# Performance work log

Measured on AMD Instinct MI355X. Metric: run time of the kernel, lower is better.

## Reference

```python
import jax, jax.numpy as jnp
import numpy as np

B, H, W = 4, 256, 256
DIM = 180
NH = 6
WH, WW = 16, 16          # window size
BH, BW = 8, 8            # base window size
CH = DIM // (2 * NH)     # per-head dim = 15
SCALE = float(CH)        # note: divide by head_dim (not sqrt), as in source
RH, RW = WH // BH, WW // BW
R = RH * RW              # spatial reduction ratio = 4
L = WH * WW              # 256 tokens per window
BL = BH * BW             # 64 base tokens
POS_DIM = (DIM // 4) // 4  # 11


def _rel_index(Hs, Ws):
    coords = np.stack(np.meshgrid(np.arange(Hs), np.arange(Ws), indexing='ij')).reshape(2, -1)
    rel = (coords[:, :, None] - coords[:, None, :]).transpose(1, 2, 0)
    rel[..., 0] += Hs - 1
    rel[..., 1] += Ws - 1
    rel[..., 0] *= 2 * Ws - 1
    return rel.sum(-1)  # (L, L) int

RPI = _rel_index(WH, WW)


def _ln(x, g, b):
    mu = x.mean(-1, keepdims=True)
    var = ((x - mu) ** 2).mean(-1, keepdims=True)
    return (x - mu) / jnp.sqrt(var + 1e-5) * g + b


def _conv(x, w, b):  # x: NHWC, w: HWIO
    y = jax.lax.conv_general_dilated(x, w, (1, 1), 'SAME',
                                     dimension_numbers=('NHWC', 'HWIO', 'NHWC'))
    return y + b


def setup_inputs():
    key = jax.random.key(0)
    ks = jax.random.split(key, 12)
    def wgt(k, shape, s=0.05):
        return jax.random.normal(k, shape, jnp.float32) * s
    C5 = DIM // 5
    d = {}
    d['x'] = jax.random.normal(ks[0], (B, H, W, DIM), jnp.float32)
    d['dfe_c1_w'] = wgt(ks[1], (1, 1, DIM, C5)); d['dfe_c1_b'] = jnp.zeros((C5,), jnp.float32)
    d['dfe_c2_w'] = wgt(ks[2], (3, 3, C5, C5));  d['dfe_c2_b'] = jnp.zeros((C5,), jnp.float32)
    d['dfe_c3_w'] = wgt(ks[3], (1, 1, C5, DIM)); d['dfe_c3_b'] = jnp.zeros((DIM,), jnp.float32)
    d['dfe_lin_w'] = wgt(ks[4], (1, 1, DIM, DIM)); d['dfe_lin_b'] = jnp.zeros((DIM,), jnp.float32)
    d['sl_w'] = wgt(ks[5], (1, R), 0.5); d['sl_b'] = jnp.zeros((1,), jnp.float32)
    d['pos_proj_w'] = wgt(ks[6], (POS_DIM, 2), 0.1); d['pos_proj_b'] = jnp.zeros((POS_DIM,), jnp.float32)
    for i, kk in zip((1, 2), (ks[7], ks[8])):
        d['pos%d_ln_g' % i] = jnp.ones((POS_DIM,), jnp.float32)
        d['pos%d_ln_b' % i] = jnp.zeros((POS_DIM,), jnp.float32)
        d['pos%d_w' % i] = wgt(kk, (POS_DIM, POS_DIM), 0.1)
        d['pos%d_b' % i] = jnp.zeros((POS_DIM,), jnp.float32)
    d['pos3_ln_g'] = jnp.ones((POS_DIM,), jnp.float32)
    d['pos3_ln_b'] = jnp.zeros((POS_DIM,), jnp.float32)
    d['pos3_w'] = wgt(ks[9], (NH, POS_DIM), 0.1)
    d['pos3_b'] = jnp.zeros((NH,), jnp.float32)
    d['proj_w'] = wgt(ks[10], (DIM, DIM))
    d['proj_b'] = jnp.zeros((DIM,), jnp.float32)
    return d


def reference(x, dfe_c1_w, dfe_c1_b, dfe_c2_w, dfe_c2_b, dfe_c3_w, dfe_c3_b,
              dfe_lin_w, dfe_lin_b, sl_w, sl_b, pos_proj_w, pos_proj_b,
              pos1_ln_g, pos1_ln_b, pos1_w, pos1_b,
              pos2_ln_g, pos2_ln_b, pos2_w, pos2_b,
              pos3_ln_g, pos3_ln_b, pos3_w, pos3_b,
              proj_w, proj_b):
    Bb, Hh, Ww_, C = x.shape
    # ---- DFE: qv = conv_path(x) * linear_path(x) ----
    t = jax.nn.leaky_relu(_conv(x, dfe_c1_w, dfe_c1_b), 0.2)
    t = jax.nn.leaky_relu(_conv(t, dfe_c2_w, dfe_c2_b), 0.2)
    t = _conv(t, dfe_c3_w, dfe_c3_b)
    qv = t * _conv(x, dfe_lin_w, dfe_lin_b)  # (B,H,W,C)
    # ---- window partition ----
    qv = qv.reshape(Bb, Hh // WH, WH, Ww_ // WW, WW, C).transpose(0, 1, 3, 2, 4, 5)
    qv = qv.reshape(-1, L, C)                       # (B_, L, C)
    B_ = qv.shape[0]
    qv = qv.reshape(B_, L, 2, NH, CH)
    q = qv[:, :, 0].transpose(0, 2, 1, 3)           # (B_, NH, L, CH)
    v = qv[:, :, 1].transpose(0, 2, 1, 3)           # (B_, NH, L, CH)
    # ---- spatial linear projection of v to base window ----
    vp = v.reshape(B_, NH, BH, RH, BW, RW, CH).transpose(0, 1, 2, 4, 6, 3, 5)
    vp = vp.reshape(B_, NH, BL, CH, R)
    vp = jnp.einsum('bnlcr,r->bnlc', vp, sl_w[0]) + sl_b[0]  # (B_, NH, BL, CH)
    # ---- spatial self-correlation ----
    corr = jnp.einsum('bnlc,bnmc->bnlm', q, vp) / SCALE       # (B_, NH, L, BL)
    # dynamic relative position bias (non-residual MLP)
    ph = jnp.arange(1 - WH, WH)
    pw = jnp.arange(1 - WW, WW)
    biases = jnp.stack(jnp.meshgrid(ph, pw, indexing='ij')).reshape(2, -1).T.astype(x.dtype)
    p = biases @ pos_proj_w.T + pos_proj_b
    p = jax.nn.relu(_ln(p, pos1_ln_g, pos1_ln_b)) @ pos1_w.T + pos1_b
    p = jax.nn.relu(_ln(p, pos2_ln_g, pos2_ln_b)) @ pos2_w.T + pos2_b
    pos = jax.nn.relu(_ln(p, pos3_ln_g, pos3_ln_b)) @ pos3_w.T + pos3_b  # ((2WH-1)(2WW-1), NH)
    rpb = pos[RPI.reshape(-1)].reshape(L, L, NH).transpose(2, 0, 1)      # (NH, L, L)
    rpb = rpb.reshape(NH, L, BH, RH, BW, RW).transpose(0, 1, 2, 4, 3, 5)
    rpb = rpb.reshape(NH, L, BL, R).mean(-1)                             # (NH, L, BL)
    corr = corr + rpb[None]
    x_sp = jnp.einsum('bnlm,bnmc->bnlc', corr, vp)
    x_sp = x_sp.transpose(0, 2, 1, 3).reshape(B_, L, C // 2)
    # ---- channel self-correlation (single-head) ----
    qc = q.transpose(0, 2, 1, 3).reshape(B_, L, C // 2)
    vc = v.transpose(0, 2, 1, 3).reshape(B_, L, C // 2)
    cmap = jnp.einsum('blc,bld->bcd', qc, vc) / float(L)                 # (B_, C/2, C/2)
    x_ch = jnp.einsum('bcd,bld->blc', cmap, vc)                          # (B_, L, C/2)
    # ---- window reverse + fuse ----
    def rev(a):
        c = a.shape[-1]
        a = a.reshape(Bb, Hh // WH, Ww_ // WW, WH, WW, c).transpose(0, 1, 3, 2, 4, 5)
        return a.reshape(Bb, Hh, Ww_, c)
    x_sp = rev(x_sp.reshape(B_, WH, WW, C // 2))
    x_ch = rev(x_ch.reshape(B_, WH, WW, C // 2))
    out = jnp.concatenate([x_sp, x_ch], -1) @ proj_w.T + proj_b          # (B,H,W,C)
    return out
```

## Files before the change

### kernel.cpp

```cpp
#include <hip/hip_runtime.h>

#define LEAKY(v) ((v) > 0.f ? (v) : 0.2f * (v))

__device__ __forceinline__ void ln_relu11(float* p, const float* __restrict__ g,
                                          const float* __restrict__ b) {
  float mu = 0.f;
#pragma unroll
  for (int j = 0; j < 11; ++j) mu += p[j];
  mu *= (1.f / 11.f);
  float var = 0.f;
#pragma unroll
  for (int j = 0; j < 11; ++j) { float d = p[j] - mu; var += d * d; }
  var *= (1.f / 11.f);
  float inv = 1.f / sqrtf(var + 1e-5f);
#pragma unroll
  for (int j = 0; j < 11; ++j) {
    float v = (p[j] - mu) * inv * g[j] + b[j];
    p[j] = v > 0.f ? v : 0.f;
  }
}

__global__ void pos_mlp_kernel(
    const float* __restrict__ w0, const float* __restrict__ b0,
    const float* __restrict__ g1, const float* __restrict__ be1,
    const float* __restrict__ w1, const float* __restrict__ b1,
    const float* __restrict__ g2, const float* __restrict__ be2,
    const float* __restrict__ w2, const float* __restrict__ b2,
    const float* __restrict__ g3, const float* __restrict__ be3,
    const float* __restrict__ w3, const float* __restrict__ b3,
    float* __restrict__ pos_out) {
  int r = blockIdx.x * 256 + threadIdx.x;
  if (r >= 961) return;
  float bh = (float)(r / 31 - 15);
  float bw = (float)(r % 31 - 15);
  float p[11], q[11];
#pragma unroll
  for (int j = 0; j < 11; ++j) p[j] = bh * w0[2 * j] + bw * w0[2 * j + 1] + b0[j];
  ln_relu11(p, g1, be1);
#pragma unroll
  for (int j = 0; j < 11; ++j) {
    float s = b1[j];
#pragma unroll
    for (int k = 0; k < 11; ++k) s += p[k] * w1[j * 11 + k];
    q[j] = s;
  }
  ln_relu11(q, g2, be2);
#pragma unroll
  for (int j = 0; j < 11; ++j) {
    float s = b2[j];
#pragma unroll
    for (int k = 0; k < 11; ++k) s += q[k] * w2[j * 11 + k];
    p[j] = s;
  }
  ln_relu11(p, g3, be3);
#pragma unroll
  for (int n = 0; n < 6; ++n) {
    float s = b3[n];
#pragma unroll
    for (int k = 0; k < 11; ++k) s += p[k] * w3[n * 11 + k];
    pos_out[r * 6 + n] = s;
  }
}

__global__ void rpb_kernel(const float* __restrict__ pos, float* __restrict__ rpb) {
  int o = blockIdx.x * 256 + threadIdx.x;
  int n = o >> 14;
  int l = (o >> 6) & 255;
  int m = o & 63;
  int i1 = l >> 4, j1 = l & 15;
  int bi = m >> 3, bj = m & 7;
  float s = 0.f;
#pragma unroll
  for (int rh = 0; rh < 2; ++rh)
#pragma unroll
    for (int rw = 0; rw < 2; ++rw) {
      int i2 = bi * 2 + rh, j2 = bj * 2 + rw;
      int idx = (i1 - i2 + 15) * 31 + (j1 - j2 + 15);
      s += pos[idx * 6 + n];
    }
  rpb[o] = s * 0.25f;
}

__global__ void pt_kernel(const float* __restrict__ pjw, float* __restrict__ pt) {
  int i = blockIdx.x * 256 + threadIdx.x;
  if (i >= 180 * 180) return;
  int c = i / 180, k = i % 180;
  pt[c * 180 + k] = pjw[k * 180 + c];
}

__global__ __launch_bounds__(256) void dfe1_kernel(const float* __restrict__ x,
                                                   const float* __restrict__ w1,
                                                   const float* __restrict__ b1,
                                                   float* __restrict__ t1) {
  __shared__ float xt[256][36];
  int t = threadIdx.x;
  int p0 = blockIdx.x * 256;
  float acc[36];
#pragma unroll
  for (int j = 0; j < 36; ++j) acc[j] = 0.f;
  for (int kc = 0; kc < 5; ++kc) {
    __syncthreads();
    for (int idx = t; idx < 256 * 36; idx += 256) {
      int px = idx / 36, ci = idx % 36;
      xt[px][ci] = x[(p0 + px) * 180 + kc * 36 + ci];
    }
    __syncthreads();
    for (int ci = 0; ci < 36; ++ci) {
      float v = xt[t][ci];
      const float* wr = &w1[(kc * 36 + ci) * 36];
#pragma unroll
      for (int j = 0; j < 36; ++j) acc[j] += v * wr[j];
    }
  }
  float* o = &t1[(p0 + t) * 36];
#pragma unroll
  for (int j = 0; j < 36; ++j) {
    float v = acc[j] + b1[j];
    o[j] = LEAKY(v);
  }
}

__global__ __launch_bounds__(256) void dfe2_kernel(const float* __restrict__ t1,
                                                   const float* __restrict__ w2,
                                                   const float* __restrict__ b2,
                                                   float* __restrict__ t2) {
  __shared__ float halo[18][18][36];
  int t = threadIdx.x;
  int blk = blockIdx.x;
  int img = blk >> 8;
  int rem = blk & 255;
  int ty0 = (rem >> 4) << 4;
  int tx0 = (rem & 15) << 4;
  for (int idx = t; idx < 18 * 18 * 36; idx += 256) {
    int ci = idx % 36;
    int xx = (idx / 36) % 18;
    int yy = idx / (36 * 18);
    int gy = ty0 + yy - 1;
    int gx = tx0 + xx - 1;
    float v = 0.f;
    if (gy >= 0 && gy < 256 && gx >= 0 && gx < 256)
      v = t1[((img * 256 + gy) * 256 + gx) * 36 + ci];
    halo[yy][xx][ci] = v;
  }
  __syncthreads();
  int ly = t >> 4, lx = t & 15;
  float acc[36];
#pragma unroll
  for (int j = 0; j < 36; ++j) acc[j] = 0.f;
#pragma unroll
  for (int kh = 0; kh < 3; ++kh)
#pragma unroll
    for (int kw = 0; kw < 3; ++kw) {
      for (int ci = 0; ci < 36; ++ci) {
        float v = halo[ly + kh][lx + kw][ci];
        const float* wr = &w2[((kh * 3 + kw) * 36 + ci) * 36];
#pragma unroll
        for (int j = 0; j < 36; ++j) acc[j] += v * wr[j];
      }
    }
  float* o = &t2[((img * 256 + ty0 + ly) * 256 + tx0 + lx) * 36];
#pragma unroll
  for (int j = 0; j < 36; ++j) {
    float v = acc[j] + b2[j];
    o[j] = LEAKY(v);
  }
}

__global__ __launch_bounds__(256, 2) void dfe3_kernel(const float* __restrict__ x,
                                                      const float* __restrict__ t2,
                                                      const float* __restrict__ w3,
                                                      const float* __restrict__ b3,
                                                      const float* __restrict__ wl,
                                                      const float* __restrict__ bl,
                                                      float* __restrict__ qv) {
  __shared__ __align__(16) float As[36 * 132];
  __shared__ __align__(16) float Bs[36 * 180 + 16];
  int t = threadIdx.x;
  int tx = t & 15;
  int ty = t >> 4;
  int p0 = blockIdx.x * 128;

  int pA0 = t / 9,           cA0 = t - pA0 * 9;
  int pA1 = (t + 256) / 9,   cA1 = (t + 256) - pA1 * 9;
  int pA2 = (t + 512) / 9,   cA2 = (t + 512) - pA2 * 9;
  int pA3 = (t + 768) / 9,   cA3 = (t + 768) - pA3 * 9;
  int pA4 = (t + 1024) / 9,  cA4 = (t + 1024) - pA4 * 9;
  const float4* xf4  = (const float4*)x;
  const float4* t2f4 = (const float4*)t2;
  const float4* wlf4 = (const float4*)wl;
  const float4* w3f4 = (const float4*)w3;
  float4* Bs4 = (float4*)Bs;

  float4 a0, a1, a2, a3, a4;
  float4 bF0, bF1, bF2, bF3, bF4, bF5, bF6;
  a4 = make_float4(0.f, 0.f, 0.f, 0.f);
  bF6 = make_float4(0.f, 0.f, 0.f, 0.f);

  auto scatterA = [&](int pa, int ca, float4 v) {
    As[(ca * 4 + 0) * 132 + pa] = v.x;
    As[(ca * 4 + 1) * 132 + pa] = v.y;
    As[(ca * 4 + 2) * 132 + pa] = v.z;
    As[(ca * 4 + 3) * 132 + pa] = v.w;
  };
  auto stage_write = [&]() {
    scatterA(pA0, cA0, a0);
    scatterA(pA1, cA1, a1);
    scatterA(pA2, cA2, a2);
    scatterA(pA3, cA3, a3);
    if (t < 128) scatterA(pA4, cA4, a4);
    Bs4[t] = bF0;
    Bs4[t + 256] = bF1;
    Bs4[t + 512] = bF2;
    Bs4[t + 768] = bF3;
    Bs4[t + 1024] = bF4;
    Bs4[t + 1280] = bF5;
    if (t < 84) Bs4[t + 1536] = bF6;
  };

  auto issue_lin = [&](int kc) {
    int kb = kc * 9;
    a0 = xf4[(size_t)(p0 + pA0) * 45 + kb + cA0];
    a1 = xf4[(size_t)(p0 + pA1) * 45 + kb + cA1];
    a2 = xf4[(size_t)(p0 + pA2) * 45 + kb + cA2];
    a3 = xf4[(size_t)(p0 + pA3) * 45 + kb + cA3];
    if (t < 128) a4 = xf4[(size_t)(p0 + pA4) * 45 + kb + cA4];
    int kw = kc * 1620;
    bF0 = wlf4[kw + t];
    bF1 = wlf4[kw + t + 256];
    bF2 = wlf4[kw + t + 512];
    bF3 = wlf4[kw + t + 768];
    bF4 = wlf4[kw + t + 1024];
    bF5 = wlf4[kw + t + 1280];
    if (t < 84) bF6 = wlf4[kw + t + 1536];
  };
  auto issue_conv = [&]() {
    a0 = t2f4[(size_t)(p0 + pA0) * 9 + cA0];
    a1 = t2f4[(size_t)(p0 + pA1) * 9 + cA1];
    a2 = t2f4[(size_t)(p0 + pA2) * 9 + cA2];
    a3 = t2f4[(size_t)(p0 + pA3) * 9 + cA3];
    if (t < 128) a4 = t2f4[(size_t)(p0 + pA4) * 9 + cA4];
    bF0 = w3f4[t];
    bF1 = w3f4[t + 256];
    bF2 = w3f4[t + 512];
    bF3 = w3f4[t + 768];
    bF4 = w3f4[t + 1024];
    bF5 = w3f4[t + 1280];
    if (t < 84) bF6 = w3f4[t + 1536];
  };

  auto compute36 = [&](float acc[8][12]) {
    for (int ci = 0; ci < 36; ++ci) {
      const float4* ap = (const float4*)&As[ci * 132 + ty * 8];
      float4 A0 = ap[0], A1 = ap[1];
      const float* bp = &Bs[ci * 180 + tx * 12];
      float4 B0 = *(const float4*)bp;
      float4 B1 = *(const float4*)(bp + 4);
      float4 B2 = *(const float4*)(bp + 8);
      float av[8] = {A0.x, A0.y, A0.z, A0.w, A1.x, A1.y, A1.z, A1.w};
      float bv[12] = {B0.x, B0.y, B0.z, B0.w, B1.x, B1.y, B1.z, B1.w,
                      B2.x, B2.y, B2.z, B2.w};
#pragma unroll
      for (int r = 0; r < 8; ++r)
#pragma unroll
        for (int j = 0; j < 12; ++j) acc[r][j] += av[r] * bv[j];
    }
  };

  issue_lin(0);
  float accL[8][12];
#pragma unroll
  for (int r = 0; r < 8; ++r)
#pragma unroll
    for (int j = 0; j < 12; ++j) accL[r][j] = 0.f;

#pragma unroll 1
  for (int p = 0; p < 5; ++p) {
    stage_write();
    __syncthreads();
    if (p < 4) issue_lin(p + 1); else issue_conv();
    compute36(accL);
    __syncthreads();
  }

  if (tx < 15) {
#pragma unroll
    for (int r = 0; r < 8; ++r) {
      int base = (p0 + ty * 8 + r) * 180 + tx * 12;
#pragma unroll
      for (int j = 0; j < 12; ++j) qv[base + j] = accL[r][j] + bl[tx * 12 + j];
    }
  }

  float accC[8][12];
#pragma unroll
  for (int r = 0; r < 8; ++r)
#pragma unroll
    for (int j = 0; j < 12; ++j) accC[r][j] = 0.f;
  stage_write();
  __syncthreads();
  compute36(accC);

  if (tx < 15) {
#pragma unroll
    for (int r = 0; r < 8; ++r) {
      int base = (p0 + ty * 8 + r) * 180 + tx * 12;
#pragma unroll
      for (int j = 0; j < 12; ++j) {
        float lp = qv[base + j];
        qv[base + j] = (accC[r][j] + b3[tx * 12 + j]) * lp;
      }
    }
  }
}

__global__ __launch_bounds__(256, 4) void att_sp_kernel(
    const float* __restrict__ qv, const float* __restrict__ slw,
    const float* __restrict__ slb, const float* __restrict__ rpb,
    const float* __restrict__ pt, const float* __restrict__ pb,
    float* __restrict__ out) {
  __shared__ __align__(16) float vp[6][64][16];
  __shared__ float xsp[128][91];
  __shared__ __align__(16) float G[6][15][16];
  int t = threadIdx.x;
  int wb = blockIdx.x;
  int b = wb >> 8, wi = (wb >> 4) & 15, wj = wb & 15;
  int wbase = (b * 256 + wi * 16) * 256 + wj * 16;
  float wsl0 = slw[0], wsl1 = slw[1], wsl2 = slw[2], wsl3 = slw[3];
  float bsl = slb[0];

  for (int idx = t; idx < 6 * 64 * 16; idx += 256) {
    int n = idx >> 10;
    int m = (idx >> 4) & 63;
    int ch = idx & 15;
    float s = 0.f;
    if (ch < 15) {
      int bi = m >> 3, bj = m & 7;
      int pa00 = (wbase + (bi * 2) * 256 + bj * 2) * 180 + 90 + n * 15 + ch;
      s = qv[pa00] * wsl0;
      s += qv[pa00 + 180] * wsl1;
      s += qv[pa00 + 256 * 180] * wsl2;
      s += qv[pa00 + 257 * 180] * wsl3;
      s += bsl;
    }
    vp[n][m][ch] = s;
  }
  __syncthreads();

  if (t < 90) {
    int n = t / 15, i = t - n * 15;
    float acc[15];
#pragma unroll
    for (int j = 0; j < 15; ++j) acc[j] = 0.f;
#pragma unroll 4
    for (int m = 0; m < 64; ++m) {
      float vi = vp[n][m][i];
      const float4* vr = (const float4*)(&vp[n][m][0]);
      float4 v0 = vr[0], v1 = vr[1], v2 = vr[2], v3 = vr[3];
      acc[0] += vi * v0.x; acc[1] += vi * v0.y; acc[2] += vi * v0.z; acc[3] += vi * v0.w;
      acc[4] += vi * v1.x; acc[5] += vi * v1.y; acc[6] += vi * v1.z; acc[7] += vi * v1.w;
      acc[8] += vi * v2.x; acc[9] += vi * v2.y; acc[10] += vi * v2.z; acc[11] += vi * v2.w;
      acc[12] += vi * v3.x; acc[13] += vi * v3.y; acc[14] += vi * v3.z;
    }
#pragma unroll
    for (int j = 0; j < 15; ++j) G[n][i][j] = acc[j];
    G[n][i][15] = 0.f;
  }
  __syncthreads();

  int lt = t & 127;
  int hg = t >> 7;
  const float inv15 = 1.f / 15.f;

#pragma unroll 1
  for (int half = 0; half < 2; ++half) {
    int l = half * 128 + lt;
    int pa = (wbase + (l >> 4) * 256 + (l & 15)) * 180;
#pragma unroll 1
    for (int nn = 0; nn < 3; ++nn) {
      int n = hg * 3 + nn;
      float qh[15];
#pragma unroll
      for (int c = 0; c < 15; ++c) qh[c] = qv[pa + n * 15 + c] * inv15;
      float xs[15];
#pragma unroll
      for (int c = 0; c < 15; ++c) xs[c] = 0.f;
#pragma unroll 3
      for (int d = 0; d < 15; ++d) {
        float qd = qh[d];
        const float4* gr = (const float4*)(&G[n][d][0]);
        float4 g0 = gr[0], g1 = gr[1], g2 = gr[2], g3 = gr[3];
        xs[0] += qd * g0.x; xs[1] += qd * g0.y; xs[2] += qd * g0.z; xs[3] += qd * g0.w;
        xs[4] += qd * g1.x; xs[5] += qd * g1.y; xs[6] += qd * g1.z; xs[7] += qd * g1.w;
        xs[8] += qd * g2.x; xs[9] += qd * g2.y; xs[10] += qd * g2.z; xs[11] += qd * g2.w;
        xs[12] += qd * g3.x; xs[13] += qd * g3.y; xs[14] += qd * g3.z;
      }
      const float* rp = &rpb[(n * 256 + l) * 64];
#pragma unroll 4
      for (int m4 = 0; m4 < 16; ++m4) {
        float4 rpv = *(const float4*)(rp + m4 * 4);
        float rparr[4] = {rpv.x, rpv.y, rpv.z, rpv.w};
#pragma unroll
        for (int mm = 0; mm < 4; ++mm) {
          const float4* vr = (const float4*)(&vp[n][m4 * 4 + mm][0]);
          float4 v0 = vr[0], v1 = vr[1], v2 = vr[2], v3 = vr[3];
          float s = rparr[mm];
          xs[0] += s * v0.x; xs[1] += s * v0.y; xs[2] += s * v0.z; xs[3] += s * v0.w;
          xs[4] += s * v1.x; xs[5] += s * v1.y; xs[6] += s * v1.z; xs[7] += s * v1.w;
          xs[8] += s * v2.x; xs[9] += s * v2.y; xs[10] += s * v2.z; xs[11] += s * v2.w;
          xs[12] += s * v3.x; xs[13] += s * v3.y; xs[14] += s * v3.z;
        }
      }
#pragma unroll
      for (int c = 0; c < 15; ++c) xsp[lt][n * 15 + c] = xs[c];
    }
    __syncthreads();
    {
      int lane = t & 63;
      int w4 = __builtin_amdgcn_readfirstlane(t >> 6);
      int k0 = w4 * 45;
      const float* ptb = pt + k0;
#pragma unroll 1
      for (int tok2 = 0; tok2 < 2; ++tok2) {
        int tt = tok2 * 64 + lane;
        int l2 = half * 128 + tt;
        int pa2 = (wbase + (l2 >> 4) * 256 + (l2 & 15)) * 180 + k0;
        float pacc[45];
#pragma unroll
        for (int j = 0; j < 45; ++j) pacc[j] = pb[k0 + j];
#pragma unroll 2
        for (int c = 0; c < 90; ++c) {
          float xv = xsp[tt][c];
          const float* prw = ptb + c * 180;
#pragma unroll
          for (int j = 0; j < 45; ++j) pacc[j] += xv * prw[j];
        }
        float* op = out + pa2;
#pragma unroll
        for (int j = 0; j < 45; ++j) op[j] = pacc[j];
      }
    }
    __syncthreads();
  }
}

__global__ __launch_bounds__(256, 2) void cmapM_kernel(const float* __restrict__ qv,
                                                       const float* __restrict__ p2t,
                                                       float* __restrict__ M) {
  __shared__ float cmt[90][91];
  __shared__ float bufA[32][97];
  __shared__ float vtt[32][97];
  int t = threadIdx.x;
  int wb = blockIdx.x;
  int b = wb >> 8, wi = (wb >> 4) & 15, wj = wb & 15;
  int wbase = (b * 256 + wi * 16) * 256 + wj * 16;

  int tx = t & 15, ty = t >> 4;
  float acc[6][6];
#pragma unroll
  for (int i = 0; i < 6; ++i)
#pragma unroll
    for (int j = 0; j < 6; ++j) acc[i][j] = 0.f;

#pragma unroll 1
  for (int ck = 0; ck < 8; ++ck) {
    __syncthreads();
    for (int idx = t; idx < 32 * 97; idx += 256) {
      int l = idx / 97, c = idx % 97;
      int gl = ck * 32 + l;
      int pa = (wbase + (gl >> 4) * 256 + (gl & 15)) * 180;
      bufA[l][c] = (c < 90) ? qv[pa + c] : 0.f;
      vtt[l][c] = (c < 90) ? qv[pa + 90 + c] : 0.f;
    }
    __syncthreads();
    for (int lk = 0; lk < 32; ++lk) {
      float aa[6], bb[6];
#pragma unroll
      for (int i = 0; i < 6; ++i) aa[i] = bufA[lk][tx * 6 + i];
#pragma unroll
      for (int j = 0; j < 6; ++j) bb[j] = vtt[lk][ty * 6 + j];
#pragma unroll
      for (int i = 0; i < 6; ++i)
#pragma unroll
        for (int j = 0; j < 6; ++j) acc[i][j] += aa[i] * bb[j];
    }
  }
  __syncthreads();
  if (tx < 15 && ty < 15) {
#pragma unroll
    for (int i = 0; i < 6; ++i)
#pragma unroll
      for (int j = 0; j < 6; ++j) cmt[tx * 6 + i][ty * 6 + j] = acc[i][j] * (1.f / 256.f);
  }
  __syncthreads();

  int lane = t & 63;
  int kq = __builtin_amdgcn_readfirstlane(t >> 6);
  int k0 = kq * 45;
  int d0 = lane;
  int d1 = lane + 64;
  int d1c = (d1 < 90) ? d1 : 0;
  float m0[45], m1[45];
#pragma unroll
  for (int j = 0; j < 45; ++j) { m0[j] = 0.f; m1[j] = 0.f; }
#pragma unroll 1
  for (int c = 0; c < 90; ++c) {
    const float* pr = p2t + c * 180 + k0;
    float v0 = cmt[c][d0];
    float v1 = cmt[c][d1c];
#pragma unroll
    for (int j = 0; j < 45; ++j) {
      float p = pr[j];
      m0[j] += p * v0;
      m1[j] += p * v1;
    }
  }
  float* M0 = M + (size_t)wb * 16200 + d0 * 180 + k0;
#pragma unroll
  for (int j = 0; j < 45; ++j) M0[j] = m0[j];
  if (d1 < 90) {
    float* M1 = M + (size_t)wb * 16200 + d1 * 180 + k0;
#pragma unroll
    for (int j = 0; j < 45; ++j) M1[j] = m1[j];
  }
}

__global__ __launch_bounds__(256, 4) void chupd_kernel(const float* __restrict__ qv,
                                                       const float* __restrict__ M,
                                                       float* __restrict__ out) {
  __shared__ float vt[64][91];
  int bid = blockIdx.x;
  int wb = bid >> 2, grp = bid & 3;
  int b = wb >> 8, wi = (wb >> 4) & 15, wj = wb & 15;
  int wbase = (b * 256 + wi * 16) * 256 + wj * 16;
  int t = threadIdx.x;

  for (int idx = t; idx < 64 * 90; idx += 256) {
    int l = idx / 90, d = idx - l * 90;
    int gl = grp * 64 + l;
    int pa = (wbase + (gl >> 4) * 256 + (gl & 15)) * 180;
    vt[l][d] = qv[pa + 90 + d];
  }
  __syncthreads();

  int l = t & 63;
  int kq = __builtin_amdgcn_readfirstlane(t >> 6);
  int k0 = kq * 45;
  const float* Mw = M + (size_t)wb * 16200;
  float pacc[45];
#pragma unroll
  for (int j = 0; j < 45; ++j) pacc[j] = 0.f;
#pragma unroll 2
  for (int d = 0; d < 90; ++d) {
    const float* mr = Mw + d * 180 + k0;
    float vl = vt[l][d];
#pragma unroll
    for (int j = 0; j < 45; ++j) pacc[j] += mr[j] * vl;
  }
  int gl = grp * 64 + l;
  int pa = (wbase + (gl >> 4) * 256 + (gl & 15)) * 180 + k0;
#pragma unroll
  for (int j = 0; j < 45; ++j) out[pa + j] += pacc[j];
}

extern "C" void kernel_launch(void* const* d_in, const int* in_sizes, int n_in,
                              void* d_out, int out_size, void* d_ws, size_t ws_size,
                              hipStream_t stream) {
  (void)in_sizes; (void)n_in; (void)out_size; (void)ws_size;
  const float* x   = (const float*)d_in[0];
  const float* w1  = (const float*)d_in[1];
  const float* b1  = (const float*)d_in[2];
  const float* w2  = (const float*)d_in[3];
  const float* b2  = (const float*)d_in[4];
  const float* w3  = (const float*)d_in[5];
  const float* b3  = (const float*)d_in[6];
  const float* wl  = (const float*)d_in[7];
  const float* bl  = (const float*)d_in[8];
  const float* slw = (const float*)d_in[9];
  const float* slb = (const float*)d_in[10];
  const float* pw0 = (const float*)d_in[11];
  const float* pb0 = (const float*)d_in[12];
  const float* g1  = (const float*)d_in[13];
  const float* be1 = (const float*)d_in[14];
  const float* mw1 = (const float*)d_in[15];
  const float* mb1 = (const float*)d_in[16];
  const float* g2  = (const float*)d_in[17];
  const float* be2 = (const float*)d_in[18];
  const float* mw2 = (const float*)d_in[19];
  const float* mb2 = (const float*)d_in[20];
  const float* g3  = (const float*)d_in[21];
  const float* be3 = (const float*)d_in[22];
  const float* mw3 = (const float*)d_in[23];
  const float* mb3 = (const float*)d_in[24];
  const float* pjw = (const float*)d_in[25];
  const float* pjb = (const float*)d_in[26];
  float* out = (float*)d_out;
  float* ws  = (float*)d_ws;

  float* qv  = ws;
  float* t1  = ws + 47185920;
  float* t2  = t1 + 9437184;
  float* pos = t2 + 9437184;
  float* rpb = pos + 5768;
  float* M   = t1;
  float* pt  = t1 + 18874368 - 32768;

  pos_mlp_kernel<<<4, 256, 0, stream>>>(pw0, pb0, g1, be1, mw1, mb1,
                                        g2, be2, mw2, mb2, g3, be3, mw3, mb3, pos);
  rpb_kernel<<<384, 256, 0, stream>>>(pos, rpb);
  dfe1_kernel<<<1024, 256, 0, stream>>>(x, w1, b1, t1);
  dfe2_kernel<<<1024, 256, 0, stream>>>(t1, w2, b2, t2);
  dfe3_kernel<<<2048, 256, 0, stream>>>(x, t2, w3, b3, wl, bl, qv);
  pt_kernel<<<127, 256, 0, stream>>>(pjw, pt);
  att_sp_kernel<<<1024, 256, 0, stream>>>(qv, slw, slb, rpb, pt, pjb, out);
  cmapM_kernel<<<1024, 256, 0, stream>>>(qv, pt + 90 * 180, M);
  chupd_kernel<<<4096, 256, 0, stream>>>(qv, M, out);
}
```

Measured before the change: 1.338 ms.

## Double dfe3 pixel tile to 256 per block and drop register prefetch

The dfe3 GEMM kernel now handles 256 pixels per block instead of 128, and each thread accumulates a 16x12 output tile instead of 8x12. This halves the grid and the number of times each block reloads the weight tiles, and raises the FMA work per shared-memory load. The register-staged software prefetch is removed, so global loads are no longer overlapped with compute, and one accumulator array is reused for both GEMMs. The 192-float accumulator plus larger staging arrays raise register pressure under launch_bounds(256,2), with a risk of spills or lower occupancy.

```diff
diff --git a/kernel.cpp b/kernel.cpp
--- a/kernel.cpp
+++ b/kernel.cpp
@@ -173,141 +173,130 @@
                                                       const float* __restrict__ wl,
                                                       const float* __restrict__ bl,
                                                       float* __restrict__ qv) {
-  __shared__ __align__(16) float As[36 * 132];
+  __shared__ __align__(16) float As[36 * 260];
   __shared__ __align__(16) float Bs[36 * 180 + 16];
   int t = threadIdx.x;
   int tx = t & 15;
   int ty = t >> 4;
-  int p0 = blockIdx.x * 128;
-
-  int pA0 = t / 9,           cA0 = t - pA0 * 9;
-  int pA1 = (t + 256) / 9,   cA1 = (t + 256) - pA1 * 9;
-  int pA2 = (t + 512) / 9,   cA2 = (t + 512) - pA2 * 9;
-  int pA3 = (t + 768) / 9,   cA3 = (t + 768) - pA3 * 9;
-  int pA4 = (t + 1024) / 9,  cA4 = (t + 1024) - pA4 * 9;
+  int p0 = blockIdx.x * 256;
+
   const float4* xf4  = (const float4*)x;
   const float4* t2f4 = (const float4*)t2;
   const float4* wlf4 = (const float4*)wl;
   const float4* w3f4 = (const float4*)w3;
   float4* Bs4 = (float4*)Bs;
 
-  float4 a0, a1, a2, a3, a4;
-  float4 bF0, bF1, bF2, bF3, bF4, bF5, bF6;
-  a4 = make_float4(0.f, 0.f, 0.f, 0.f);
-  bF6 = make_float4(0.f, 0.f, 0.f, 0.f);
-
-  auto scatterA = [&](int pa, int ca, float4 v) {
-    As[(ca * 4 + 0) * 132 + pa] = v.x;
-    As[(ca * 4 + 1) * 132 + pa] = v.y;
-    As[(ca * 4 + 2) * 132 + pa] = v.z;
-    As[(ca * 4 + 3) * 132 + pa] = v.w;
+  auto stageA_x = [&](int kb) {
+    float4 r[9];
+#pragma unroll
+    for (int c = 0; c < 9; ++c) {
+      int idx = t + c * 256;
+      int px = idx / 9, ca = idx - px * 9;
+      r[c] = xf4[(size_t)(p0 + px) * 45 + kb + ca];
+    }
+#pragma unroll
+    for (int c = 0; c < 9; ++c) {
+      int idx = t + c * 256;
+      int px = idx / 9, ca = idx - px * 9;
+      As[(ca * 4 + 0) * 260 + px] = r[c].x;
+      As[(ca * 4 + 1) * 260 + px] = r[c].y;
+      As[(ca * 4 + 2) * 260 + px] = r[c].z;
+      As[(ca * 4 + 3) * 260 + px] = r[c].w;
+    }
   };
-  auto stage_write = [&]() {
-    scatterA(pA0, cA0, a0);
-    scatterA(pA1, cA1, a1);
-    scatterA(pA2, cA2, a2);
-    scatterA(pA3, cA3, a3);
-    if (t < 128) scatterA(pA4, cA4, a4);
-    Bs4[t] = bF0;
-    Bs4[t + 256] = bF1;
-    Bs4[t + 512] = bF2;
-    Bs4[t + 768] = bF3;
-    Bs4[t + 1024] = bF4;
-    Bs4[t + 1280] = bF5;
-    if (t < 84) Bs4[t + 1536] = bF6;
+  auto stageA_t2 = [&]() {
+    float4 r[9];
+#pragma unroll
+    for (int c = 0; c < 9; ++c) {
+      int idx = t + c * 256;
+      int px = idx / 9, ca = idx - px * 9;
+      r[c] = t2f4[(size_t)(p0 + px) * 9 + ca];
+    }
+#pragma unroll
+    for (int c = 0; c < 9; ++c) {
+      int idx = t + c * 256;
+      int px = idx / 9, ca = idx - px * 9;
+      As[(ca * 4 + 0) * 260 + px] = r[c].x;
+      As[(ca * 4 + 1) * 260 + px] = r[c].y;
+      As[(ca * 4 + 2) * 260 + px] = r[c].z;
+      As[(ca * 4 + 3) * 260 + px] = r[c].w;
+    }
   };
-
-  auto issue_lin = [&](int kc) {
-    int kb = kc * 9;
-    a0 = xf4[(size_t)(p0 + pA0) * 45 + kb + cA0];
-    a1 = xf4[(size_t)(p0 + pA1) * 45 + kb + cA1];
-    a2 = xf4[(size_t)(p0 + pA2) * 45 + kb + cA2];
-    a3 = xf4[(size_t)(p0 + pA3) * 45 + kb + cA3];
-    if (t < 128) a4 = xf4[(size_t)(p0 + pA4) * 45 + kb + cA4];
-    int kw = kc * 1620;
-    bF0 = wlf4[kw + t];
-    bF1 = wlf4[kw + t + 256];
-    bF2 = wlf4[kw + t + 512];
-    bF3 = wlf4[kw + t + 768];
-    bF4 = wlf4[kw + t + 1024];
-    bF5 = wlf4[kw + t + 1280];
-    if (t < 84) bF6 = wlf4[kw + t + 1536];
+  auto stageB = [&](const float4* src, int kw) {
+    float4 r[7];
+#pragma unroll
+    for (int c = 0; c < 7; ++c) {
+      int idx = t + c * 256;
+      if (idx < 1620) r[c] = src[kw + idx];
+    }
+#pragma unroll
+    for (int c = 0; c < 7; ++c) {
+      int idx = t + c * 256;
+      if (idx < 1620) Bs4[idx] = r[c];
+    }
   };
-  auto issue_conv = [&]() {
-    a0 = t2f4[(size_t)(p0 + pA0) * 9 + cA0];
-    a1 = t2f4[(size_t)(p0 + pA1) * 9 + cA1];
-    a2 = t2f4[(size_t)(p0 + pA2) * 9 + cA2];
-    a3 = t2f4[(size_t)(p0 + pA3) * 9 + cA3];
-    if (t < 128) a4 = t2f4[(size_t)(p0 + pA4) * 9 + cA4];
-    bF0 = w3f4[t];
-    bF1 = w3f4[t + 256];
-    bF2 = w3f4[t + 512];
-    bF3 = w3f4[t + 768];
-    bF4 = w3f4[t + 1024];
-    bF5 = w3f4[t + 1280];
-    if (t < 84) bF6 = w3f4[t + 1536];
-  };
-
-  auto compute36 = [&](float acc[8][12]) {
+
+  auto compute36 = [&](float acc[16][12]) {
     for (int ci = 0; ci < 36; ++ci) {
-      const float4* ap = (const float4*)&As[ci * 132 + ty * 8];
-      float4 A0 = ap[0], A1 = ap[1];
+      const float4* ap = (const float4*)&As[ci * 260 + ty * 16];
+      float4 A0 = ap[0], A1 = ap[1], A2 = ap[2], A3 = ap[3];
       const float* bp = &Bs[ci * 180 + tx * 12];
       float4 B0 = *(const float4*)bp;
       float4 B1 = *(const float4*)(bp + 4);
       float4 B2 = *(const float4*)(bp + 8);
-      float av[8] = {A0.x, A0.y, A0.z, A0.w, A1.x, A1.y, A1.z, A1.w};
+      float av[16] = {A0.x, A0.y, A0.z, A0.w, A1.x, A1.y, A1.z, A1.w,
+                      A2.x, A2.y, A2.z, A2.w, A3.x, A3.y, A3.z, A3.w};
       float bv[12] = {B0.x, B0.y, B0.z, B0.w, B1.x, B1.y, B1.z, B1.w,
                       B2.x, B2.y, B2.z, B2.w};
 #pragma unroll
-      for (int r = 0; r < 8; ++r)
+      for (int r = 0; r < 16; ++r)
 #pragma unroll
         for (int j = 0; j < 12; ++j) acc[r][j] += av[r] * bv[j];
     }
   };
 
-  issue_lin(0);
-  float accL[8][12];
-#pragma unroll
-  for (int r = 0; r < 8; ++r)
-#pragma unroll
-    for (int j = 0; j < 12; ++j) accL[r][j] = 0.f;
+  float acc[16][12];
+#pragma unroll
+  for (int r = 0; r < 16; ++r)
+#pragma unroll
+    for (int j = 0; j < 12; ++j) acc[r][j] = 0.f;
 
 #pragma unroll 1
   for (int p = 0; p < 5; ++p) {
-    stage_write();
-    __syncthreads();
-    if (p < 4) issue_lin(p + 1); else issue_conv();
-    compute36(accL);
-    __syncthreads();
+    __syncthreads();
+    stageA_x(p * 9);
+    stageB(wlf4, p * 1620);
+    __syncthreads();
+    compute36(acc);
   }
 
   if (tx < 15) {
 #pragma unroll
-    for (int r = 0; r < 8; ++r) {
-      int base = (p0 + ty * 8 + r) * 180 + tx * 12;
-#pragma unroll
-      for (int j = 0; j < 12; ++j) qv[base + j] = accL[r][j] + bl[tx * 12 + j];
-    }
-  }
-
-  float accC[8][12];
-#pragma unroll
-  for (int r = 0; r < 8; ++r)
-#pragma unroll
-    for (int j = 0; j < 12; ++j) accC[r][j] = 0.f;
-  stage_write();
-  __syncthreads();
-  compute36(accC);
+    for (int r = 0; r < 16; ++r) {
+      int base = (p0 + ty * 16 + r) * 180 + tx * 12;
+#pragma unroll
+      for (int j = 0; j < 12; ++j) qv[base + j] = acc[r][j] + bl[tx * 12 + j];
+    }
+  }
+
+#pragma unroll
+  for (int r = 0; r < 16; ++r)
+#pragma unroll
+    for (int j = 0; j < 12; ++j) acc[r][j] = 0.f;
+  __syncthreads();
+  stageA_t2();
+  stageB(w3f4, 0);
+  __syncthreads();
+  compute36(acc);
 
   if (tx < 15) {
 #pragma unroll
-    for (int r = 0; r < 8; ++r) {
-      int base = (p0 + ty * 8 + r) * 180 + tx * 12;
+    for (int r = 0; r < 16; ++r) {
+      int base = (p0 + ty * 16 + r) * 180 + tx * 12;
 #pragma unroll
       for (int j = 0; j < 12; ++j) {
         float lp = qv[base + j];
-        qv[base + j] = (accC[r][j] + b3[tx * 12 + j]) * lp;
+        qv[base + j] = (acc[r][j] + b3[tx * 12 + j]) * lp;
       }
     }
   }
@@ -609,7 +598,7 @@
   rpb_kernel<<<384, 256, 0, stream>>>(pos, rpb);
   dfe1_kernel<<<1024, 256, 0, stream>>>(x, w1, b1, t1);
   dfe2_kernel<<<1024, 256, 0, stream>>>(t1, w2, b2, t2);
-  dfe3_kernel<<<2048, 256, 0, stream>>>(x, t2, w3, b3, wl, bl, qv);
+  dfe3_kernel<<<1024, 256, 0, stream>>>(x, t2, w3, b3, wl, bl, qv);
   pt_kernel<<<127, 256, 0, stream>>>(pjw, pt);
   att_sp_kernel<<<1024, 256, 0, stream>>>(qv, slw, slb, rpb, pt, pjb, out);
   cmapM_kernel<<<1024, 256, 0, stream>>>(qv, pt + 90 * 180, M);
```

New measurement: 1.445 ms. +8.0%, slower.

## Split A staging into two halves to cut LDS and registers in dfe3

Applied to the files above, without the earlier changes.

The dfe3 GEMM kernel now stages the A tile in two sub-chunks of 16 and 20 channels instead of all 36 at once. This shrinks the As shared buffer and the per-thread prefetch registers, and a single accumulator array is reused for the linear and conv passes. Launch bounds are raised from 2 to 3 blocks per CU to exploit the lower resource use. The cost is twice as many barriers per k-step and a less complete overlap of global loads with compute.

```diff
diff --git a/kernel.cpp b/kernel.cpp
--- a/kernel.cpp
+++ b/kernel.cpp
@@ -166,48 +166,53 @@
   }
 }
 
-__global__ __launch_bounds__(256, 2) void dfe3_kernel(const float* __restrict__ x,
+__global__ __launch_bounds__(256, 3) void dfe3_kernel(const float* __restrict__ x,
                                                       const float* __restrict__ t2,
                                                       const float* __restrict__ w3,
                                                       const float* __restrict__ b3,
                                                       const float* __restrict__ wl,
                                                       const float* __restrict__ bl,
                                                       float* __restrict__ qv) {
-  __shared__ __align__(16) float As[36 * 132];
+  __shared__ __align__(16) float As[20 * 132];
   __shared__ __align__(16) float Bs[36 * 180 + 16];
   int t = threadIdx.x;
   int tx = t & 15;
   int ty = t >> 4;
   int p0 = blockIdx.x * 128;
 
-  int pA0 = t / 9,           cA0 = t - pA0 * 9;
-  int pA1 = (t + 256) / 9,   cA1 = (t + 256) - pA1 * 9;
-  int pA2 = (t + 512) / 9,   cA2 = (t + 512) - pA2 * 9;
-  int pA3 = (t + 768) / 9,   cA3 = (t + 768) - pA3 * 9;
-  int pA4 = (t + 1024) / 9,  cA4 = (t + 1024) - pA4 * 9;
+  int pH0a = t >> 2,          cH0a = t & 3;
+  int pH0b = (t + 256) >> 2,  cH0b = (t + 256) & 3;
+  int pH1a = t / 5,           cH1a = t % 5;
+  int pH1b = (t + 256) / 5,   cH1b = (t + 256) % 5;
+  int pH1c = (t + 512) / 5,   cH1c = (t + 512) % 5;
+
   const float4* xf4  = (const float4*)x;
   const float4* t2f4 = (const float4*)t2;
   const float4* wlf4 = (const float4*)wl;
   const float4* w3f4 = (const float4*)w3;
   float4* Bs4 = (float4*)Bs;
 
-  float4 a0, a1, a2, a3, a4;
+  float4 a0, a1, a2;
   float4 bF0, bF1, bF2, bF3, bF4, bF5, bF6;
-  a4 = make_float4(0.f, 0.f, 0.f, 0.f);
+  a2 = make_float4(0.f, 0.f, 0.f, 0.f);
   bF6 = make_float4(0.f, 0.f, 0.f, 0.f);
 
-  auto scatterA = [&](int pa, int ca, float4 v) {
-    As[(ca * 4 + 0) * 132 + pa] = v.x;
-    As[(ca * 4 + 1) * 132 + pa] = v.y;
-    As[(ca * 4 + 2) * 132 + pa] = v.z;
-    As[(ca * 4 + 3) * 132 + pa] = v.w;
-  };
-  auto stage_write = [&]() {
-    scatterA(pA0, cA0, a0);
-    scatterA(pA1, cA1, a1);
-    scatterA(pA2, cA2, a2);
-    scatterA(pA3, cA3, a3);
-    if (t < 128) scatterA(pA4, cA4, a4);
+  auto scatterA = [&](int row, int pa, float4 v) {
+    As[(row + 0) * 132 + pa] = v.x;
+    As[(row + 1) * 132 + pa] = v.y;
+    As[(row + 2) * 132 + pa] = v.z;
+    As[(row + 3) * 132 + pa] = v.w;
+  };
+  auto writeAh0 = [&]() {
+    scatterA(cH0a * 4, pH0a, a0);
+    scatterA(cH0b * 4, pH0b, a1);
+  };
+  auto writeAh1 = [&]() {
+    scatterA(cH1a * 4, pH1a, a0);
+    scatterA(cH1b * 4, pH1b, a1);
+    if (t < 128) scatterA(cH1c * 4, pH1c, a2);
+  };
+  auto writeB = [&]() {
     Bs4[t] = bF0;
     Bs4[t + 256] = bF1;
     Bs4[t + 512] = bF2;
@@ -217,42 +222,45 @@
     if (t < 84) Bs4[t + 1536] = bF6;
   };
 
-  auto issue_lin = [&](int kc) {
-    int kb = kc * 9;
-    a0 = xf4[(size_t)(p0 + pA0) * 45 + kb + cA0];
-    a1 = xf4[(size_t)(p0 + pA1) * 45 + kb + cA1];
-    a2 = xf4[(size_t)(p0 + pA2) * 45 + kb + cA2];
-    a3 = xf4[(size_t)(p0 + pA3) * 45 + kb + cA3];
-    if (t < 128) a4 = xf4[(size_t)(p0 + pA4) * 45 + kb + cA4];
-    int kw = kc * 1620;
-    bF0 = wlf4[kw + t];
-    bF1 = wlf4[kw + t + 256];
-    bF2 = wlf4[kw + t + 512];
-    bF3 = wlf4[kw + t + 768];
-    bF4 = wlf4[kw + t + 1024];
-    bF5 = wlf4[kw + t + 1280];
-    if (t < 84) bF6 = wlf4[kw + t + 1536];
-  };
-  auto issue_conv = [&]() {
-    a0 = t2f4[(size_t)(p0 + pA0) * 9 + cA0];
-    a1 = t2f4[(size_t)(p0 + pA1) * 9 + cA1];
-    a2 = t2f4[(size_t)(p0 + pA2) * 9 + cA2];
-    a3 = t2f4[(size_t)(p0 + pA3) * 9 + cA3];
-    if (t < 128) a4 = t2f4[(size_t)(p0 + pA4) * 9 + cA4];
-    bF0 = w3f4[t];
-    bF1 = w3f4[t + 256];
-    bF2 = w3f4[t + 512];
-    bF3 = w3f4[t + 768];
-    bF4 = w3f4[t + 1024];
-    bF5 = w3f4[t + 1280];
-    if (t < 84) bF6 = w3f4[t + 1536];
-  };
-
-  auto compute36 = [&](float acc[8][12]) {
-    for (int ci = 0; ci < 36; ++ci) {
+  auto issueB = [&](const float4* src, int kw) {
+    bF0 = src[kw + t];
+    bF1 = src[kw + t + 256];
+    bF2 = src[kw + t + 512];
+    bF3 = src[kw + t + 768];
+    bF4 = src[kw + t + 1024];
+    bF5 = src[kw + t + 1280];
+    if (t < 84) bF6 = src[kw + t + 1536];
+  };
+  auto issueAh0_x = [&](int kb) {
+    a0 = xf4[(size_t)(p0 + pH0a) * 45 + kb + cH0a];
+    a1 = xf4[(size_t)(p0 + pH0b) * 45 + kb + cH0b];
+  };
+  auto issueAh1_x = [&](int kb) {
+    a0 = xf4[(size_t)(p0 + pH1a) * 45 + kb + 4 + cH1a];
+    a1 = xf4[(size_t)(p0 + pH1b) * 45 + kb + 4 + cH1b];
+    if (t < 128) a2 = xf4[(size_t)(p0 + pH1c) * 45 + kb + 4 + cH1c];
+  };
+  auto issueAh0_t2 = [&]() {
+    a0 = t2f4[(size_t)(p0 + pH0a) * 9 + cH0a];
+    a1 = t2f4[(size_t)(p0 + pH0b) * 9 + cH0b];
+  };
+  auto issueAh1_t2 = [&]() {
+    a0 = t2f4[(size_t)(p0 + pH1a) * 9 + 4 + cH1a];
+    a1 = t2f4[(size_t)(p0 + pH1b) * 9 + 4 + cH1b];
+    if (t < 128) a2 = t2f4[(size_t)(p0 + pH1c) * 9 + 4 + cH1c];
+  };
+
+  float acc[8][12];
+#pragma unroll
+  for (int r = 0; r < 8; ++r)
+#pragma unroll
+    for (int j = 0; j < 12; ++j) acc[r][j] = 0.f;
+
+  auto compute = [&](int nci, int hbase) {
+    for (int ci = 0; ci < nci; ++ci) {
       const float4* ap = (const float4*)&As[ci * 132 + ty * 8];
       float4 A0 = ap[0], A1 = ap[1];
-      const float* bp = &Bs[ci * 180 + tx * 12];
+      const float* bp = &Bs[(hbase + ci) * 180 + tx * 12];
       float4 B0 = *(const float4*)bp;
       float4 B1 = *(const float4*)(bp + 4);
       float4 B2 = *(const float4*)(bp + 8);
@@ -266,20 +274,23 @@
     }
   };
 
-  issue_lin(0);
-  float accL[8][12];
-#pragma unroll
-  for (int r = 0; r < 8; ++r)
-#pragma unroll
-    for (int j = 0; j < 12; ++j) accL[r][j] = 0.f;
+  issueB(wlf4, 0);
+  issueAh0_x(0);
 
 #pragma unroll 1
   for (int p = 0; p < 5; ++p) {
-    stage_write();
-    __syncthreads();
-    if (p < 4) issue_lin(p + 1); else issue_conv();
-    compute36(accL);
-    __syncthreads();
+    __syncthreads();
+    writeB();
+    writeAh0();
+    __syncthreads();
+    issueAh1_x(p * 9);
+    compute(16, 0);
+    __syncthreads();
+    writeAh1();
+    __syncthreads();
+    if (p < 4) { issueB(wlf4, (p + 1) * 1620); issueAh0_x((p + 1) * 9); }
+    else       { issueB(w3f4, 0);              issueAh0_t2(); }
+    compute(20, 16);
   }
 
   if (tx < 15) {
@@ -287,18 +298,24 @@
     for (int r = 0; r < 8; ++r) {
       int base = (p0 + ty * 8 + r) * 180 + tx * 12;
 #pragma unroll
-      for (int j = 0; j < 12; ++j) qv[base + j] = accL[r][j] + bl[tx * 12 + j];
-    }
-  }
-
-  float accC[8][12];
+      for (int j = 0; j < 12; ++j) qv[base + j] = acc[r][j] + bl[tx * 12 + j];
+    }
+  }
+
 #pragma unroll
   for (int r = 0; r < 8; ++r)
 #pragma unroll
-    for (int j = 0; j < 12; ++j) accC[r][j] = 0.f;
-  stage_write();
-  __syncthreads();
-  compute36(accC);
+    for (int j = 0; j < 12; ++j) acc[r][j] = 0.f;
+  __syncthreads();
+  writeB();
+  writeAh0();
+  __syncthreads();
+  issueAh1_t2();
+  compute(16, 0);
+  __syncthreads();
+  writeAh1();
+  __syncthreads();
+  compute(20, 16);
 
   if (tx < 15) {
 #pragma unroll
@@ -307,7 +324,7 @@
 #pragma unroll
       for (int j = 0; j < 12; ++j) {
         float lp = qv[base + j];
-        qv[base + j] = (accC[r][j] + b3[tx * 12 + j]) * lp;
+        qv[base + j] = (acc[r][j] + b3[tx * 12 + j]) * lp;
       }
     }
   }
```

Result: slower. 1.415 ms (+5.8%).
